# Kernel optimization log

Measured on AMD Instinct MI355X. Metric: run time of the kernel, lower is better.

Reference implementation:

```python
import jax, jax.numpy as jnp
import numpy as np

NUM_HEADS = 16
HEAD_DIM = 64
D_MODEL = NUM_HEADS * HEAD_DIM  # 1024
B, L = 512, 64


def setup_inputs() -> dict:
    key = jax.random.key(0)
    ks = jax.random.split(key, 6)
    s = 1.0 / np.sqrt(D_MODEL)
    x = jax.random.normal(ks[0], (B, L, D_MODEL), dtype=jnp.float32)
    bias = jax.random.normal(ks[1], (1, NUM_HEADS, L, L), dtype=jnp.float32)
    Wq = jax.random.normal(ks[2], (D_MODEL, NUM_HEADS * HEAD_DIM), dtype=jnp.float32) * s
    Wk = jax.random.normal(ks[3], (D_MODEL, NUM_HEADS * HEAD_DIM), dtype=jnp.float32) * s
    Wv = jax.random.normal(ks[4], (D_MODEL, NUM_HEADS * HEAD_DIM), dtype=jnp.float32) * s
    Wo = jax.random.normal(ks[5], (NUM_HEADS * HEAD_DIM, D_MODEL), dtype=jnp.float32) * s
    return {"x": x, "bias": bias, "Wq": Wq, "Wk": Wk, "Wv": Wv, "Wo": Wo}


def reference(x, bias, Wq, Wk, Wv, Wo):
    Bsz, Ls, D = x.shape
    H, Dh = NUM_HEADS, HEAD_DIM
    # QKV projections (no bias), reshape to [B, H, L, Dh]
    q = (x @ Wq).reshape(Bsz, Ls, H, Dh).transpose(0, 2, 1, 3)
    k = (x @ Wk).reshape(Bsz, Ls, H, Dh).transpose(0, 2, 1, 3)
    v = (x @ Wv).reshape(Bsz, Ls, H, Dh).transpose(0, 2, 1, 3)
    scale = jnp.sqrt(jnp.float32(Dh))
    # [B, H, L, L]
    attn_logits = jnp.einsum('bhqd,bhkd->bhqk', q, k) / scale + bias
    attn_weights = jax.nn.softmax(attn_logits, axis=-1)
    # weighted sum -> [B, L, H*Dh]
    out = jnp.einsum('bhqk,bhkd->bhqd', attn_weights, v)
    out = out.transpose(0, 2, 1, 3).reshape(Bsz, Ls, H * Dh)
    return out @ Wo
```

## Files before the change

### kernel.cpp

```cpp
#include <hip/hip_runtime.h>
#include <hip/hip_bf16.h>
#include <stdint.h>

__device__ inline float bf2f(ushort u) {
    union { uint32_t u; float f; } v; v.u = ((uint32_t)u) << 16; return v.f;
}
__device__ inline ushort f2bf(float f) {
    union { float f; uint32_t u; } v; v.f = f;
    uint32_t u = v.u;
    uint32_t r = (u + 0x7fffu + ((u >> 16) & 1u)) >> 16;
    return (ushort)r;
}
__device__ inline uint32_t pk2bf(uint32_t flo, uint32_t fhi) {
    uint32_t lo = (flo + 0x7fffu + ((flo >> 16) & 1u)) >> 16;
    uint32_t hi = (fhi + 0x7fffu + ((fhi >> 16) & 1u)) >> 16;
    return lo | (hi << 16);
}

typedef __attribute__((ext_vector_type(8))) short bf16x8;
typedef __attribute__((ext_vector_type(4))) float f32x4;

__device__ inline void gload_lds16(const ushort* g, ushort* l) {
    __builtin_amdgcn_global_load_lds(
        (const __attribute__((address_space(1))) void*)g,
        (__attribute__((address_space(3))) void*)l, 16, 0, 0);
}

__global__ void transpose1024(const float* __restrict__ Wq, const float* __restrict__ Wk,
                              const float* __restrict__ Wv, const float* __restrict__ Wo,
                              ushort* __restrict__ WqT, ushort* __restrict__ WkT,
                              ushort* __restrict__ WvT, ushort* __restrict__ WoT) {
    const float* in; ushort* out;
    switch (blockIdx.z) {
        case 0: in = Wq; out = WqT; break;
        case 1: in = Wk; out = WkT; break;
        case 2: in = Wv; out = WvT; break;
        default: in = Wo; out = WoT; break;
    }
    __shared__ ushort tile[64][65];
    const int t = threadIdx.x;
    const int c = t & 63, rq = t >> 6;
    const int bx = blockIdx.x * 64, by = blockIdx.y * 64;
#pragma unroll
    for (int i = 0; i < 16; ++i) {
        int r = i * 4 + rq;
        tile[r][c] = f2bf(in[(size_t)(by + r) * 1024 + bx + c]);
    }
    __syncthreads();
#pragma unroll
    for (int i = 0; i < 16; ++i) {
        int r = i * 4 + rq;
        out[(size_t)(bx + r) * 1024 + by + c] = tile[c][r];
    }
}

__global__ __launch_bounds__(256)
void cast_bf16(const float* __restrict__ in, ushort* __restrict__ out, size_t n8) {
    size_t i = (size_t)blockIdx.x * blockDim.x + threadIdx.x;
    const size_t stride = (size_t)gridDim.x * blockDim.x;
    for (; i < n8; i += stride) {
        const uint4 lo = *(const uint4*)&in[i * 8];
        const uint4 hi = *(const uint4*)&in[i * 8 + 4];
        uint4 o;
        o.x = pk2bf(lo.x, lo.y); o.y = pk2bf(lo.z, lo.w);
        o.z = pk2bf(hi.x, hi.y); o.w = pk2bf(hi.z, hi.w);
        *(uint4*)&out[i * 8] = o;
    }
}

template <bool C_F32>
__global__ __launch_bounds__(512, 2)
void gemm256(const ushort* __restrict__ A, int lda, const ushort* __restrict__ Bt,
             void* __restrict__ C_, int M, int N, int K) {
    __shared__ __attribute__((aligned(16))) ushort lds[65536];
    const int t = threadIdx.x;
    const int lane = t & 63, wave = t >> 6;
    const int wm = wave >> 2, wn = wave & 3;
    const int quad = lane >> 4, l16 = lane & 15;

    const int gx = N >> 8;
    const int nwg = gridDim.x * gridDim.y;
    int wg = blockIdx.y * gridDim.x + blockIdx.x;
    {
        const int q = nwg >> 3, r = nwg & 7;
        const int xcd = wg & 7, loc = wg >> 3;
        wg = (xcd < r ? xcd * (q + 1) : r * (q + 1) + (xcd - r) * q) + loc;
    }
    const int m0 = (wg / gx) << 8, n0 = (wg % gx) << 8;

    const f32x4 zero = {0.f, 0.f, 0.f, 0.f};
    f32x4 acc[8][4];
#pragma unroll
    for (int i = 0; i < 8; ++i)
#pragma unroll
        for (int j = 0; j < 4; ++j) acc[i][j] = zero;

    auto STAGE = [&](const ushort* __restrict__ src, int ldb, int rc0, int kcol,
                     int regio, int buf) {
        ushort* l = &lds[buf * 32768 + regio];
#pragma unroll
        for (int j = 0; j < 2; ++j) {
            const int g = j * 512 + t;
            const int r = g >> 3;
            const int cg = (((g & 7) ^ (r & 7)) * 8);
            gload_lds16(&src[(size_t)(rc0 + r) * ldb + kcol + cg],
                        &l[(j * 512 + wave * 64) * 8]);
        }
    };
    auto LOFF = [&](int R, int gq) { return R * 64 + ((gq ^ (R & 7)) * 8); };

    const int NT = K >> 6;
    const int abase = wm * 8192;
    const int bbase = 16384 + (wn >> 1) * 8192;
    const int brow = (wn & 1) * 64;

    STAGE(A, lda, m0, 0, 0, 0);
    STAGE(A, lda, m0 + 128, 0, 8192, 0);
    STAGE(Bt, K, n0, 0, 16384, 0);
    STAGE(Bt, K, n0 + 128, 0, 24576, 0);
    asm volatile("s_waitcnt vmcnt(0)" ::: "memory");
    __builtin_amdgcn_s_barrier();

    int cur = 0;
    for (int kt = 0; kt < NT; ++kt) {
        const bool nx = kt + 1 < NT;
        const int kn = (kt + 1) << 6;
        const ushort* la = &lds[cur * 32768 + abase];
        const ushort* lb = &lds[cur * 32768 + bbase];
        bf16x8 af[4], bf[4];

        if (nx) STAGE(A, lda, m0, kn, 0, cur ^ 1);
        if (kt > 0) {
            if (nx) asm volatile("s_waitcnt vmcnt(2)" ::: "memory");
            else    asm volatile("s_waitcnt vmcnt(0)" ::: "memory");
        }
        __builtin_amdgcn_s_barrier();
#pragma unroll
        for (int i = 0; i < 4; ++i) {
            af[i] = *(const bf16x8*)&la[LOFF(i * 16 + l16, quad)];
            bf[i] = *(const bf16x8*)&lb[LOFF(brow + i * 16 + l16, quad)];
        }
        __builtin_amdgcn_s_setprio(1);
#pragma unroll
        for (int i = 0; i < 4; ++i)
#pragma unroll
            for (int n = 0; n < 4; ++n)
                acc[i][n] = __builtin_amdgcn_mfma_f32_16x16x32_bf16(af[i], bf[n], acc[i][n], 0, 0, 0);
        __builtin_amdgcn_s_setprio(0);
        __builtin_amdgcn_s_barrier();

#pragma unroll
        for (int i = 0; i < 4; ++i)
            af[i] = *(const bf16x8*)&la[LOFF((i + 4) * 16 + l16, quad)];
        if (nx) STAGE(A, lda, m0 + 128, kn, 8192, cur ^ 1);
        __builtin_amdgcn_s_barrier();
        __builtin_amdgcn_s_setprio(1);
#pragma unroll
        for (int i = 0; i < 4; ++i)
#pragma unroll
            for (int n = 0; n < 4; ++n)
                acc[i + 4][n] = __builtin_amdgcn_mfma_f32_16x16x32_bf16(af[i], bf[n], acc[i + 4][n], 0, 0, 0);
        __builtin_amdgcn_s_setprio(0);
        __builtin_amdgcn_s_barrier();

#pragma unroll
        for (int i = 0; i < 4; ++i) {
            af[i] = *(const bf16x8*)&la[LOFF(i * 16 + l16, 4 + quad)];
            bf[i] = *(const bf16x8*)&lb[LOFF(brow + i * 16 + l16, 4 + quad)];
        }
        if (nx) STAGE(Bt, K, n0, kn, 16384, cur ^ 1);
        __builtin_amdgcn_s_barrier();
        __builtin_amdgcn_s_setprio(1);
#pragma unroll
        for (int i = 0; i < 4; ++i)
#pragma unroll
            for (int n = 0; n < 4; ++n)
                acc[i][n] = __builtin_amdgcn_mfma_f32_16x16x32_bf16(af[i], bf[n], acc[i][n], 0, 0, 0);
        __builtin_amdgcn_s_setprio(0);
        __builtin_amdgcn_s_barrier();

#pragma unroll
        for (int i = 0; i < 4; ++i)
            af[i] = *(const bf16x8*)&la[LOFF((i + 4) * 16 + l16, 4 + quad)];
        if (nx) STAGE(Bt, K, n0 + 128, kn, 24576, cur ^ 1);
        __builtin_amdgcn_s_barrier();
        __builtin_amdgcn_s_setprio(1);
#pragma unroll
        for (int i = 0; i < 4; ++i)
#pragma unroll
            for (int n = 0; n < 4; ++n)
                acc[i + 4][n] = __builtin_amdgcn_mfma_f32_16x16x32_bf16(af[i], bf[n], acc[i + 4][n], 0, 0, 0);
        __builtin_amdgcn_s_setprio(0);
        __builtin_amdgcn_s_barrier();

        cur ^= 1;
    }

#pragma unroll
    for (int mt = 0; mt < 8; ++mt)
#pragma unroll
        for (int nt = 0; nt < 4; ++nt)
#pragma unroll
            for (int r4 = 0; r4 < 4; ++r4) {
                const int row = m0 + wm * 128 + mt * 16 + quad * 4 + r4;
                const int col = n0 + wn * 64 + nt * 16 + l16;
                if (C_F32) ((float*)C_)[(size_t)row * N + col] = acc[mt][nt][r4];
                else       ((ushort*)C_)[(size_t)row * N + col] = f2bf(acc[mt][nt][r4]);
            }
}

__global__ __launch_bounds__(256)
void attn_mfma(ushort* __restrict__ QK, const ushort* __restrict__ Vt,
               const float* __restrict__ bias, int CROWS) {
    const int t = threadIdx.x;
    const int lane = t & 63, wave = t >> 6;
    const int quad = lane >> 4, l16 = lane & 15;
    const int b = blockIdx.x >> 4, h = blockIdx.x & 15;
    const int SQK = 2048;
    const size_t qbase = (size_t)b * 64 * SQK + (size_t)h * 64;
    const size_t kbase = qbase + 1024;
    const size_t vbase = (size_t)(h * 64) * CROWS + (size_t)b * 64;

    __shared__ __attribute__((aligned(16))) ushort Pl[4 * 16 * 72];

    bf16x8 qf[2];
#pragma unroll
    for (int ks = 0; ks < 2; ++ks)
        qf[ks] = *(const bf16x8*)&QK[qbase + (size_t)(wave * 16 + l16) * SQK + ks * 32 + quad * 8];

    const f32x4 zero = {0.f, 0.f, 0.f, 0.f};
    f32x4 s[4];
#pragma unroll
    for (int nt = 0; nt < 4; ++nt) s[nt] = zero;
#pragma unroll
    for (int nt = 0; nt < 4; ++nt)
#pragma unroll
        for (int ks = 0; ks < 2; ++ks) {
            bf16x8 kf = *(const bf16x8*)&QK[kbase + (size_t)(nt * 16 + l16) * SQK + ks * 32 + quad * 8];
            s[nt] = __builtin_amdgcn_mfma_f32_16x16x32_bf16(qf[ks], kf, s[nt], 0, 0, 0);
        }

    const int q0 = wave * 16 + quad * 4;
    float p[4][4];
#pragma unroll
    for (int nt = 0; nt < 4; ++nt)
#pragma unroll
        for (int r4 = 0; r4 < 4; ++r4)
            p[nt][r4] = s[nt][r4] * 0.125f +
                        bias[(size_t)(h * 64 + q0 + r4) * 64 + nt * 16 + l16];

    float rinv[4];
#pragma unroll
    for (int r4 = 0; r4 < 4; ++r4) {
        float m = fmaxf(fmaxf(p[0][r4], p[1][r4]), fmaxf(p[2][r4], p[3][r4]));
        m = fmaxf(m, __shfl_xor(m, 1));
        m = fmaxf(m, __shfl_xor(m, 2));
        m = fmaxf(m, __shfl_xor(m, 4));
        m = fmaxf(m, __shfl_xor(m, 8));
#pragma unroll
        for (int nt = 0; nt < 4; ++nt) p[nt][r4] = __expf(p[nt][r4] - m);
        float sum = p[0][r4] + p[1][r4] + p[2][r4] + p[3][r4];
        sum += __shfl_xor(sum, 1);
        sum += __shfl_xor(sum, 2);
        sum += __shfl_xor(sum, 4);
        sum += __shfl_xor(sum, 8);
        rinv[r4] = 1.f / sum;
    }

#pragma unroll
    for (int nt = 0; nt < 4; ++nt)
#pragma unroll
        for (int r4 = 0; r4 < 4; ++r4)
            Pl[(wave * 16 + quad * 4 + r4) * 72 + nt * 16 + l16] = f2bf(p[nt][r4]);
    __syncthreads();

    bf16x8 pa[2];
#pragma unroll
    for (int ks = 0; ks < 2; ++ks)
        pa[ks] = *(const bf16x8*)&Pl[(wave * 16 + l16) * 72 + ks * 32 + quad * 8];
    f32x4 o[4];
#pragma unroll
    for (int nt = 0; nt < 4; ++nt) o[nt] = zero;
#pragma unroll
    for (int nt = 0; nt < 4; ++nt)
#pragma unroll
        for (int ks = 0; ks < 2; ++ks) {
            bf16x8 vf = *(const bf16x8*)&Vt[vbase + (size_t)(nt * 16 + l16) * CROWS + ks * 32 + quad * 8];
            o[nt] = __builtin_amdgcn_mfma_f32_16x16x32_bf16(pa[ks], vf, o[nt], 0, 0, 0);
        }

#pragma unroll
    for (int nt = 0; nt < 4; ++nt)
#pragma unroll
        for (int r4 = 0; r4 < 4; ++r4)
            QK[qbase + (size_t)(q0 + r4) * SQK + nt * 16 + l16] = f2bf(o[nt][r4] * rinv[r4]);
}

extern "C" void kernel_launch(void* const* d_in, const int* in_sizes, int n_in,
                              void* d_out, int out_size, void* d_ws, size_t ws_size,
                              hipStream_t stream) {
    const float* x    = (const float*)d_in[0];
    const float* bias = (const float*)d_in[1];
    const float* Wq   = (const float*)d_in[2];
    const float* Wk   = (const float*)d_in[3];
    const float* Wv   = (const float*)d_in[4];
    const float* Wo   = (const float*)d_in[5];
    float* out = (float*)d_out;

    const size_t D = 1024;
    const size_t WB = 4 * D * D * 2;

    int CHUNK_B = 128;
    if (ws_size >= WB + (size_t)512 * 64 * 6144)      CHUNK_B = 512;
    else if (ws_size >= WB + (size_t)256 * 64 * 6144) CHUNK_B = 256;
    const int NCHUNK = 512 / CHUNK_B;
    const size_t CROWS = (size_t)CHUNK_B * 64;
    const size_t CELEM = CROWS * D;

    ushort* WqT = (ushort*)d_ws;
    ushort* WkT = WqT + D * D;
    ushort* WvT = WkT + D * D;
    ushort* WoT = WvT + D * D;
    ushort* QKc = WoT + D * D;
    ushort* Vtc = QKc + CROWS * 2048;

    transpose1024<<<dim3(16, 16, 4), 256, 0, stream>>>(Wq, Wk, Wv, Wo, WqT, WkT, WvT, WoT);

    for (int c = 0; c < NCHUNK; ++c) {
        const float* xc = x + (size_t)c * CELEM;
        float* outc = out + (size_t)c * CELEM;
        ushort* Xc = (ushort*)outc;
        cast_bf16<<<2048, 256, 0, stream>>>(xc, Xc, CELEM / 8);
        gemm256<false><<<dim3(8, CROWS / 256), 512, 0, stream>>>(
            Xc, 1024, WqT, QKc, (int)CROWS, 2048, 1024);
        gemm256<false><<<dim3(CROWS / 256, 4), 512, 0, stream>>>(
            WvT, 1024, Xc, Vtc, 1024, (int)CROWS, 1024);
        attn_mfma<<<CHUNK_B * 16, 256, 0, stream>>>(QKc, Vtc, bias, (int)CROWS);
        gemm256<true><<<dim3(4, CROWS / 256), 512, 0, stream>>>(
            QKc, 2048, WoT, outc, (int)CROWS, 1024, 1024);
    }
}
```

Baseline: 607.0 us.

## Fuse V projection into QK GEMM and transpose V in attention LDS

```diff
diff --git a/kernel.cpp b/kernel.cpp
--- a/kernel.cpp
+++ b/kernel.cpp
@@ -210,23 +210,30 @@
 }
 
 __global__ __launch_bounds__(256)
-void attn_mfma(ushort* __restrict__ QK, const ushort* __restrict__ Vt,
-               const float* __restrict__ bias, int CROWS) {
+void attn_mfma(ushort* __restrict__ QKV, const float* __restrict__ bias, int CROWS) {
     const int t = threadIdx.x;
     const int lane = t & 63, wave = t >> 6;
     const int quad = lane >> 4, l16 = lane & 15;
     const int b = blockIdx.x >> 4, h = blockIdx.x & 15;
-    const int SQK = 2048;
+    const int SQK = 3072;
     const size_t qbase = (size_t)b * 64 * SQK + (size_t)h * 64;
     const size_t kbase = qbase + 1024;
-    const size_t vbase = (size_t)(h * 64) * CROWS + (size_t)b * 64;
 
     __shared__ __attribute__((aligned(16))) ushort Pl[4 * 16 * 72];
+    __shared__ __attribute__((aligned(16))) ushort Vt[64 * 72];
+
+    bf16x8 vstage[2];
+#pragma unroll
+    for (int i = 0; i < 2; ++i) {
+        const int s = i * 256 + t;
+        const int tok = s >> 3, g = s & 7;
+        vstage[i] = *(const bf16x8*)&QKV[(size_t)(b * 64 + tok) * SQK + 2048 + h * 64 + g * 8];
+    }
 
     bf16x8 qf[2];
 #pragma unroll
     for (int ks = 0; ks < 2; ++ks)
-        qf[ks] = *(const bf16x8*)&QK[qbase + (size_t)(wave * 16 + l16) * SQK + ks * 32 + quad * 8];
+        qf[ks] = *(const bf16x8*)&QKV[qbase + (size_t)(wave * 16 + l16) * SQK + ks * 32 + quad * 8];
 
     const f32x4 zero = {0.f, 0.f, 0.f, 0.f};
     f32x4 s[4];
@@ -236,7 +243,7 @@
     for (int nt = 0; nt < 4; ++nt)
 #pragma unroll
         for (int ks = 0; ks < 2; ++ks) {
-            bf16x8 kf = *(const bf16x8*)&QK[kbase + (size_t)(nt * 16 + l16) * SQK + ks * 32 + quad * 8];
+            bf16x8 kf = *(const bf16x8*)&QKV[kbase + (size_t)(nt * 16 + l16) * SQK + ks * 32 + quad * 8];
             s[nt] = __builtin_amdgcn_mfma_f32_16x16x32_bf16(qf[ks], kf, s[nt], 0, 0, 0);
         }
 
@@ -272,6 +279,18 @@
 #pragma unroll
         for (int r4 = 0; r4 < 4; ++r4)
             Pl[(wave * 16 + quad * 4 + r4) * 72 + nt * 16 + l16] = f2bf(p[nt][r4]);
+
+#pragma unroll
+    for (int i = 0; i < 2; ++i) {
+        const int s = i * 256 + t;
+        const int tok = s >> 3, g = s & 7;
+#pragma unroll
+        for (int j = 0; j < 8; ++j) {
+            const int d = g * 8 + j;
+            Vt[d * 72 + (((tok >> 3) ^ ((d >> 3) & 7)) << 3) + (tok & 7)] =
+                (ushort)vstage[i][j];
+        }
+    }
     __syncthreads();
 
     bf16x8 pa[2];
@@ -285,7 +304,8 @@
     for (int nt = 0; nt < 4; ++nt)
 #pragma unroll
         for (int ks = 0; ks < 2; ++ks) {
-            bf16x8 vf = *(const bf16x8*)&Vt[vbase + (size_t)(nt * 16 + l16) * CROWS + ks * 32 + quad * 8];
+            const int d = nt * 16 + l16;
+            bf16x8 vf = *(const bf16x8*)&Vt[d * 72 + (((ks * 4 + quad) ^ ((d >> 3) & 7)) << 3)];
             o[nt] = __builtin_amdgcn_mfma_f32_16x16x32_bf16(pa[ks], vf, o[nt], 0, 0, 0);
         }
 
@@ -293,7 +313,7 @@
     for (int nt = 0; nt < 4; ++nt)
 #pragma unroll
         for (int r4 = 0; r4 < 4; ++r4)
-            QK[qbase + (size_t)(q0 + r4) * SQK + nt * 16 + l16] = f2bf(o[nt][r4] * rinv[r4]);
+            QKV[qbase + (size_t)(q0 + r4) * SQK + nt * 16 + l16] = f2bf(o[nt][r4] * rinv[r4]);
 }
 
 extern "C" void kernel_launch(void* const* d_in, const int* in_sizes, int n_in,
@@ -317,12 +337,11 @@
     const size_t CROWS = (size_t)CHUNK_B * 64;
     const size_t CELEM = CROWS * D;
 
-    ushort* WqT = (ushort*)d_ws;
-    ushort* WkT = WqT + D * D;
-    ushort* WvT = WkT + D * D;
-    ushort* WoT = WvT + D * D;
-    ushort* QKc = WoT + D * D;
-    ushort* Vtc = QKc + CROWS * 2048;
+    ushort* WqT  = (ushort*)d_ws;
+    ushort* WkT  = WqT + D * D;
+    ushort* WvT  = WkT + D * D;
+    ushort* WoT  = WvT + D * D;
+    ushort* QKVc = WoT + D * D;
 
     transpose1024<<<dim3(16, 16, 4), 256, 0, stream>>>(Wq, Wk, Wv, Wo, WqT, WkT, WvT, WoT);
 
@@ -331,12 +350,10 @@
         float* outc = out + (size_t)c * CELEM;
         ushort* Xc = (ushort*)outc;
         cast_bf16<<<2048, 256, 0, stream>>>(xc, Xc, CELEM / 8);
-        gemm256<false><<<dim3(8, CROWS / 256), 512, 0, stream>>>(
-            Xc, 1024, WqT, QKc, (int)CROWS, 2048, 1024);
-        gemm256<false><<<dim3(CROWS / 256, 4), 512, 0, stream>>>(
-            WvT, 1024, Xc, Vtc, 1024, (int)CROWS, 1024);
-        attn_mfma<<<CHUNK_B * 16, 256, 0, stream>>>(QKc, Vtc, bias, (int)CROWS);
+        gemm256<false><<<dim3(12, CROWS / 256), 512, 0, stream>>>(
+            Xc, 1024, WqT, QKVc, (int)CROWS, 3072, 1024);
+        attn_mfma<<<CHUNK_B * 16, 256, 0, stream>>>(QKVc, bias, (int)CROWS);
         gemm256<true><<<dim3(4, CROWS / 256), 512, 0, stream>>>(
-            QKc, 2048, WoT, outc, (int)CROWS, 1024, 1024);
-    }
-}
+            QKVc, 3072, WoT, outc, (int)CROWS, 1024, 1024);
+    }
+}
```

New measurement: 586.3 us. 3.4% less time.
